# Optimization experiments

Hardware: AMD Instinct MI355X
Metric: run time of the kernel (lower is better)

The kernel has to match this reference:

```python
import jax, jax.numpy as jnp
import numpy as np

TEMP = 0.5  # temperature_f from init


def setup_inputs() -> dict:
    key = jax.random.key(0)
    k1, k2, k3 = jax.random.split(key, 3)
    B, d = 4096, 128
    h_i = jax.random.normal(k1, (B, d), dtype=jnp.float32)
    h_j = jax.random.normal(k2, (B, d), dtype=jnp.float32)
    S = jax.random.uniform(k3, (B, B), dtype=jnp.float32)
    return {"h_i": h_i, "h_j": h_j, "S": S}


def reference(h_i, h_j, S):
    B = h_i.shape[0]
    N = 2 * B
    h = jnp.concatenate([h_i, h_j], axis=0)                 # [N, d]
    sim = jnp.matmul(h, h.T) / TEMP                          # [N, N]
    # S_2 = 1 - (S**2).repeat(2,2); sim1 = sim * S_2
    S2 = 1.0 - jnp.tile(S * S, (2, 2))                       # [N, N]
    sim1 = sim * S2
    # positives: diag(sim, +B) and diag(sim, -B)
    idx = jnp.arange(B)
    pos = jnp.concatenate([sim[idx, idx + B], sim[idx + B, idx]])  # [N]
    # negatives mask: exclude diagonal and the positive-pair positions
    i = jnp.arange(N)[:, None]
    j = jnp.arange(N)[None, :]
    neg_mask = ~((i == j) | (j == (i + B) % N))              # [N, N], N-2 True per row
    neg = jnp.where(neg_mask, sim1, -jnp.inf)                # masked entries drop out of logsumexp
    # CrossEntropy(label=0, reduction='sum') over logits=[pos, negatives]:
    # loss_n = logsumexp(logits_n) - pos_n  (order of negatives is irrelevant)
    logits = jnp.concatenate([pos[:, None], neg], axis=1)    # [N, N-1] effective
    lse = jax.nn.logsumexp(logits, axis=1)
    loss = jnp.sum(lse - pos) / N
    return loss
```

## Files before the change

kernel.cpp:

```cpp
#include <hip/hip_runtime.h>
#include <hip/hip_bf16.h>

#define B_ROWS 4096
#define NN     8192
#define DD     128
#define NSPLIT 64
#define NTRI   2080
#define SPA    68
#define CSHIFT 128.0f

typedef __attribute__((ext_vector_type(8))) short s8v;
typedef __attribute__((ext_vector_type(4))) float f4v;
typedef __attribute__((ext_vector_type(2))) float f2v;
typedef __attribute__((ext_vector_type(4))) unsigned short u16x4;
typedef unsigned int u32;

static constexpr float SCALE_H = 1.6986436f;
static constexpr float SCALE2  = 2.8853900818f;
static constexpr float LN2     = 0.6931471805599453f;

__device__ __forceinline__ float fast_exp2(float x) {
#if __has_builtin(__builtin_amdgcn_exp2f)
    return __builtin_amdgcn_exp2f(x);
#else
    return exp2f(x);
#endif
}

__device__ __forceinline__ unsigned short s2m_pack(float x, bool msk) {
    float s2 = msk ? 0.f : 1.f - x * x;
    union { __hip_bfloat16 h; unsigned short u; } cv;
    cv.h = __float2bfloat16(s2);
    return cv.u;
}

__device__ __forceinline__ float bf16f(unsigned short u) {
    return __uint_as_float(((u32)u) << 16);
}

typedef __attribute__((address_space(1))) const u32 gu32;
typedef __attribute__((address_space(3))) u32 lu32;
__device__ __forceinline__ void gload_lds16(const void* g, void* l) {
    __builtin_amdgcn_global_load_lds((gu32*)g, (lu32*)l, 16, 0, 0);
}

__global__ void hpos_kernel(const float* __restrict__ hi, const float* __restrict__ hj,
                            __hip_bfloat16* __restrict__ hb, float* __restrict__ pos2) {
    int w = threadIdx.x >> 6, l = threadIdx.x & 63;
    int row = blockIdx.x * 4 + w;
    f2v a = ((const f2v*)(hi + (size_t)row * DD))[l];
    f2v b = ((const f2v*)(hj + (size_t)row * DD))[l];
    float d = a[0] * b[0] + a[1] * b[1];
    #pragma unroll
    for (int off = 32; off; off >>= 1) d += __shfl_xor(d, off, 64);
    if (l == 0) pos2[row] = SCALE2 * d;
    union { ushort2 u2; __hip_bfloat16 h[2]; } ua, ub;
    ua.h[0] = __float2bfloat16(a[0] * SCALE_H);
    ua.h[1] = __float2bfloat16(a[1] * SCALE_H);
    ub.h[0] = __float2bfloat16(b[0] * SCALE_H);
    ub.h[1] = __float2bfloat16(b[1] * SCALE_H);
    ((ushort2*)(hb + (size_t)row * DD))[l] = ua.u2;
    ((ushort2*)(hb + (size_t)(row + B_ROWS) * DD))[l] = ub.u2;
}

__global__ __launch_bounds__(512, 4)
void main_kernel(const __hip_bfloat16* __restrict__ hb, const float* __restrict__ S,
                 float* __restrict__ ssplit) {
    __shared__ short ldsB[128][128];
    __shared__ unsigned short sA[64][SPA];
    __shared__ unsigned short sB[64][SPA];
    __shared__ float mrg[768];

    const int orig = blockIdx.x;
    const int bid  = (orig & 7) * (NTRI / 8) + (orig >> 3);
    int j = (int)((sqrtf(8.0f * (float)bid + 1.0f) - 1.0f) * 0.5f);
    while (((j + 1) * (j + 2)) / 2 <= bid) ++j;
    while ((j * (j + 1)) / 2 > bid) --j;
    const int i = bid - (j * (j + 1)) / 2;
    const bool diag = (i == j);

    const int tid = threadIdx.x;
    const int l  = tid & 63;
    const int w  = tid >> 6;
    const int wm = w >> 1, wn = w & 1;
    const int lc = l & 15;
    const int lk = l >> 4;
    const int r64 = i * 64, c64 = j * 64;

    const s8v* hb8 = (const s8v*)hb;

    #pragma unroll
    for (int i2 = 0; i2 < 4; i2++) {
        const int rowb = w * 16 + i2 * 4;
        const int lrw  = rowb + lk;
        const int grow = c64 + ((lrw < 64) ? lrw : (lrw - 64 + B_ROWS));
        const int sc16 = lc ^ (lrw & 7);
        gload_lds16((const char*)hb + ((size_t)grow << 8) + (sc16 << 4),
                    (char*)&ldsB[rowb][0]);
    }

    {
        const int rr = tid >> 3;
        const int c8 = (tid & 7) * 8;
        const float* gA = S + (size_t)(r64 + rr) * B_ROWS + c64 + c8;
        const float* gB = S + (size_t)(c64 + rr) * B_ROWS + r64 + c8;
        f4v a0 = ((const f4v*)gA)[0], a1 = ((const f4v*)gA)[1];
        f4v b0 = ((const f4v*)gB)[0], b1 = ((const f4v*)gB)[1];
        u16x4 pa0, pa1, pb0, pb1;
        #pragma unroll
        for (int e = 0; e < 4; e++) {
            pa0[e] = s2m_pack(a0[e], diag && (c8 + e     == rr));
            pa1[e] = s2m_pack(a1[e], diag && (c8 + 4 + e == rr));
            pb0[e] = s2m_pack(b0[e], false);
            pb1[e] = s2m_pack(b1[e], false);
        }
        *(u16x4*)&sA[rr][c8]     = pa0;
        *(u16x4*)&sA[rr][c8 + 4] = pa1;
        *(u16x4*)&sB[rr][c8]     = pb0;
        *(u16x4*)&sB[rr][c8 + 4] = pb1;
    }

    s8v afr[2][4];
    #pragma unroll
    for (int fm = 0; fm < 2; fm++) {
        int ar = (r64 + wm * 16 + lc) + fm * B_ROWS;
        #pragma unroll
        for (int kk = 0; kk < 4; kk++)
            afr[fm][kk] = hb8[ar * 16 + kk * 4 + lk];
    }
    __syncthreads();

    const char* bp[4];
    {
        const char* bb = (const char*)ldsB + (wn * 32 + lc) * 256;
        #pragma unroll
        for (int kk = 0; kk < 4; kk++)
            bp[kk] = bb + (((kk * 4 + lk) ^ (lc & 7)) << 4);
    }
    f4v acc[2][2][2];
    #pragma unroll
    for (int fm = 0; fm < 2; fm++)
        #pragma unroll
        for (int fh = 0; fh < 2; fh++)
            #pragma unroll
            for (int cg = 0; cg < 2; cg++) acc[fm][fh][cg] = f4v{0.f, 0.f, 0.f, 0.f};
    #pragma unroll
    for (int kk = 0; kk < 4; kk++) {
        #pragma unroll
        for (int fh = 0; fh < 2; fh++)
            #pragma unroll
            for (int cg = 0; cg < 2; cg++) {
                s8v bf = *(const s8v*)(bp[kk] + fh * 16384 + cg * 4096);
                acc[0][fh][cg] = __builtin_amdgcn_mfma_f32_16x16x32_bf16(
                    afr[0][kk], bf, acc[0][fh][cg], 0, 0, 0);
                acc[1][fh][cg] = __builtin_amdgcn_mfma_f32_16x16x32_bf16(
                    afr[1][kk], bf, acc[1][fh][cg], 0, 0, 0);
            }
    }

    float rsum[2][4], csum[2][2];
    #pragma unroll
    for (int fm = 0; fm < 2; fm++)
        #pragma unroll
        for (int r = 0; r < 4; r++) rsum[fm][r] = 0.f;
    csum[0][0] = csum[0][1] = csum[1][0] = csum[1][1] = 0.f;

    #pragma unroll
    for (int r = 0; r < 4; r++) {
        const int rr = wm * 16 + lk * 4 + r;
        #pragma unroll
        for (int cg = 0; cg < 2; cg++) {
            const int cc = wn * 32 + cg * 16 + lc;
            const float s2a = bf16f(sA[rr][cc]);
            const float s2b = bf16f(sB[cc][rr]);
            #pragma unroll
            for (int fm = 0; fm < 2; fm++)
                #pragma unroll
                for (int fh = 0; fh < 2; fh++) {
                    const float a = acc[fm][fh][cg][r];
                    rsum[fm][r]  += fast_exp2(fmaf(a, s2a, -CSHIFT));
                    csum[fh][cg] += fast_exp2(fmaf(a, s2b, -CSHIFT));
                }
        }
    }

    #pragma unroll
    for (int fm = 0; fm < 2; fm++) {
        #pragma unroll
        for (int r = 0; r < 4; r++) {
            float ss = rsum[fm][r];
            #pragma unroll
            for (int off = 1; off < 16; off <<= 1) ss += __shfl_xor(ss, off, 64);
            if (lc == 0) mrg[wn * 128 + fm * 64 + (wm * 16 + lk * 4 + r)] = ss;
        }
    }
    #pragma unroll
    for (int fh = 0; fh < 2; fh++) {
        #pragma unroll
        for (int cg = 0; cg < 2; cg++) {
            float ss = csum[fh][cg];
            ss += __shfl_xor(ss, 16, 64);
            ss += __shfl_xor(ss, 32, 64);
            if (l < 16) mrg[256 + wm * 128 + fh * 64 + (wn * 32 + cg * 16 + lc)] = ss;
        }
    }
    __syncthreads();

    if (tid < 128) {
        int fm = tid >> 6, rho = tid & 63;
        float v = mrg[fm * 64 + rho] + mrg[128 + fm * 64 + rho];
        ssplit[(size_t)j * NN + (r64 + rho + fm * B_ROWS)] = v;
    } else if (!diag && tid < 256) {
        int t2 = tid - 128, fh = t2 >> 6, cc = t2 & 63;
        float v = mrg[256 +   0 + fh * 64 + cc] + mrg[256 + 128 + fh * 64 + cc]
                + mrg[256 + 256 + fh * 64 + cc] + mrg[256 + 384 + fh * 64 + cc];
        ssplit[(size_t)i * NN + (c64 + cc + fh * B_ROWS)] = v;
    }
}

__global__ __launch_bounds__(256)
void reduce_kernel(const float* __restrict__ ssplit, const float* __restrict__ pos2,
                   float* __restrict__ partial) {
    __shared__ float red[256];
    const int n = blockIdx.x * 256 + threadIdx.x;
    float p = pos2[n & (B_ROWS - 1)];
    float Ssum = fast_exp2(p - CSHIFT);
    #pragma unroll 8
    for (int sp = 0; sp < NSPLIT; sp++)
        Ssum += ssplit[(size_t)sp * NN + n];
    red[threadIdx.x] = (CSHIFT + log2f(Ssum)) - p;
    __syncthreads();
    for (int st = 128; st; st >>= 1) {
        if (threadIdx.x < st) red[threadIdx.x] += red[threadIdx.x + st];
        __syncthreads();
    }
    if (threadIdx.x == 0) partial[blockIdx.x] = red[0];
}

__global__ void final_kernel(const float* __restrict__ partial, float* __restrict__ out) {
    if (threadIdx.x == 0) {
        float s = 0.f;
        #pragma unroll
        for (int i = 0; i < 32; i++) s += partial[i];
        out[0] = s * (LN2 / (float)NN);
    }
}

extern "C" void kernel_launch(void* const* d_in, const int* in_sizes, int n_in,
                              void* d_out, int out_size, void* d_ws, size_t ws_size,
                              hipStream_t stream) {
    (void)in_sizes; (void)n_in; (void)out_size; (void)ws_size;
    const float* hi = (const float*)d_in[0];
    const float* hj = (const float*)d_in[1];
    const float* S  = (const float*)d_in[2];

    char* ws = (char*)d_ws;
    __hip_bfloat16* hb = (__hip_bfloat16*)ws;
    float* pos2   = (float*)(ws + 2097152);
    float* ssplit = (float*)(ws + 2097152 + 16384);
    float* partial= (float*)(ws + 2097152 + 16384 + 2097152);

    hpos_kernel<<<1024, 256, 0, stream>>>(hi, hj, hb, pos2);
    main_kernel<<<NTRI, 512, 0, stream>>>(hb, S, ssplit);
    reduce_kernel<<<32, 256, 0, stream>>>(ssplit, pos2, partial);
    final_kernel<<<1, 64, 0, stream>>>(partial, (float*)d_out);
}
```

Measured before the change: 46.29 us.

## Alias S-tile and merge buffers onto the B tile LDS region

The S-derived scale tiles and the merge buffer now reuse the ldsB shared-memory region after the MFMA phase, instead of having their own allocations. The raw S values are kept in registers across the matmul, and packing into LDS is deferred until after an extra barrier. This cuts per-block LDS use so more blocks can be resident per CU. In exchange it adds two barriers, holds more live registers during the matmul, and serialises the S packing behind the MFMA work.

```diff
diff --git a/kernel.cpp b/kernel.cpp
--- a/kernel.cpp
+++ b/kernel.cpp
@@ -67,9 +67,6 @@
 void main_kernel(const __hip_bfloat16* __restrict__ hb, const float* __restrict__ S,
                  float* __restrict__ ssplit) {
     __shared__ short ldsB[128][128];
-    __shared__ unsigned short sA[64][SPA];
-    __shared__ unsigned short sB[64][SPA];
-    __shared__ float mrg[768];
 
     const int orig = blockIdx.x;
     const int bid  = (orig & 7) * (NTRI / 8) + (orig >> 3);
@@ -99,25 +96,14 @@
                     (char*)&ldsB[rowb][0]);
     }
 
+    const int prr = tid >> 3;
+    const int pc8 = (tid & 7) * 8;
+    f4v a0, a1, b0, b1;
     {
-        const int rr = tid >> 3;
-        const int c8 = (tid & 7) * 8;
-        const float* gA = S + (size_t)(r64 + rr) * B_ROWS + c64 + c8;
-        const float* gB = S + (size_t)(c64 + rr) * B_ROWS + r64 + c8;
-        f4v a0 = ((const f4v*)gA)[0], a1 = ((const f4v*)gA)[1];
-        f4v b0 = ((const f4v*)gB)[0], b1 = ((const f4v*)gB)[1];
-        u16x4 pa0, pa1, pb0, pb1;
-        #pragma unroll
-        for (int e = 0; e < 4; e++) {
-            pa0[e] = s2m_pack(a0[e], diag && (c8 + e     == rr));
-            pa1[e] = s2m_pack(a1[e], diag && (c8 + 4 + e == rr));
-            pb0[e] = s2m_pack(b0[e], false);
-            pb1[e] = s2m_pack(b1[e], false);
-        }
-        *(u16x4*)&sA[rr][c8]     = pa0;
-        *(u16x4*)&sA[rr][c8 + 4] = pa1;
-        *(u16x4*)&sB[rr][c8]     = pb0;
-        *(u16x4*)&sB[rr][c8 + 4] = pb1;
+        const float* gA = S + (size_t)(r64 + prr) * B_ROWS + c64 + pc8;
+        const float* gB = S + (size_t)(c64 + prr) * B_ROWS + r64 + pc8;
+        a0 = ((const f4v*)gA)[0]; a1 = ((const f4v*)gA)[1];
+        b0 = ((const f4v*)gB)[0]; b1 = ((const f4v*)gB)[1];
     }
 
     s8v afr[2][4];
@@ -128,6 +114,9 @@
         for (int kk = 0; kk < 4; kk++)
             afr[fm][kk] = hb8[ar * 16 + kk * 4 + lk];
     }
+
+    asm volatile("" : "+v"(a0), "+v"(a1), "+v"(b0), "+v"(b1) :: "memory");
+
     __syncthreads();
 
     const char* bp[4];
@@ -158,6 +147,26 @@
             }
     }
 
+    __syncthreads();
+
+    unsigned short* sAp = (unsigned short*)&ldsB[0][0];
+    unsigned short* sBp = sAp + 64 * SPA;
+    {
+        u16x4 pa0, pa1, pb0, pb1;
+        #pragma unroll
+        for (int e = 0; e < 4; e++) {
+            pa0[e] = s2m_pack(a0[e], diag && (pc8 + e     == prr));
+            pa1[e] = s2m_pack(a1[e], diag && (pc8 + 4 + e == prr));
+            pb0[e] = s2m_pack(b0[e], false);
+            pb1[e] = s2m_pack(b1[e], false);
+        }
+        *(u16x4*)&sAp[prr * SPA + pc8]     = pa0;
+        *(u16x4*)&sAp[prr * SPA + pc8 + 4] = pa1;
+        *(u16x4*)&sBp[prr * SPA + pc8]     = pb0;
+        *(u16x4*)&sBp[prr * SPA + pc8 + 4] = pb1;
+    }
+    __syncthreads();
+
     float rsum[2][4], csum[2][2];
     #pragma unroll
     for (int fm = 0; fm < 2; fm++)
@@ -171,8 +180,8 @@
         #pragma unroll
         for (int cg = 0; cg < 2; cg++) {
             const int cc = wn * 32 + cg * 16 + lc;
-            const float s2a = bf16f(sA[rr][cc]);
-            const float s2b = bf16f(sB[cc][rr]);
+            const float s2a = bf16f(sAp[rr * SPA + cc]);
+            const float s2b = bf16f(sBp[cc * SPA + rr]);
             #pragma unroll
             for (int fm = 0; fm < 2; fm++)
                 #pragma unroll
@@ -184,6 +193,7 @@
         }
     }
 
+    float* mrg = (float*)((char*)&ldsB[0][0] + 2 * 64 * SPA * 2);
     #pragma unroll
     for (int fm = 0; fm < 2; fm++) {
         #pragma unroll
```

Measured after the change: 50.97 us. 1.1x slower.
